# Kernel optimization log

Hardware: AMD Instinct MI355X
Metric: run time of the kernel (lower is better)

The kernel has to match this reference:

```python
import jax, jax.numpy as jnp
import numpy as np

B, C, L = 8, 256, 1024
N_HEAD = 8
GROUPS = 32
EPS = 1e-5


def group_norm(x, gamma, beta):
    # x: [B, C, L]
    b, c, l = x.shape
    xg = x.reshape(b, GROUPS, (c // GROUPS) * l)
    mu = xg.mean(-1, keepdims=True)
    var = xg.var(-1, keepdims=True)
    xg = (xg - mu) / jnp.sqrt(var + EPS)
    x = xg.reshape(b, c, l)
    return x * gamma[None, :, None] + beta[None, :, None]


def conv1d(x, w, b=None, groups=1):
    # x: [B,C,L], w: [O, I/groups, K]
    k = w.shape[-1]
    pad = (k - 1) // 2
    y = jax.lax.conv_general_dilated(
        x, w, window_strides=(1,), padding=[(pad, pad)],
        dimension_numbers=('NCH', 'OIH', 'NCH'),
        feature_group_count=groups)
    if b is not None:
        y = y + b[None, :, None]
    return y


def setup_inputs() -> dict:
    key = jax.random.key(0)
    ks = jax.random.split(key, 8)
    x = jax.random.normal(ks[0], (B, C, L), dtype=jnp.float32)
    gamma = jnp.ones((C,), jnp.float32)
    beta = jnp.zeros((C,), jnp.float32)
    # depthwise conv: torch weight [C,1,3], kaiming_normal fan_in=1*3
    dw_w = jax.random.normal(ks[1], (C, 1, 3), jnp.float32) * np.sqrt(2.0 / 3.0)
    # qkv 1x1 conv: [3C, C, 1], kaiming fan_in=C
    qkv_w = jax.random.normal(ks[2], (3 * C, C, 1), jnp.float32) * np.sqrt(2.0 / C)
    qkv_b = jnp.zeros((3 * C,), jnp.float32)
    out_w = jax.random.normal(ks[3], (C, C, 1), jnp.float32) * np.sqrt(2.0 / C)
    out_b = jnp.zeros((C,), jnp.float32)
    return {"x": x, "gamma": gamma, "beta": beta, "dw_w": dw_w,
            "qkv_w": qkv_w, "qkv_b": qkv_b, "out_w": out_w, "out_b": out_b}


def reference(x, gamma, beta, dw_w, qkv_w, qkv_b, out_w, out_b):
    b, c, l = x.shape
    head_dim = c // N_HEAD
    h = group_norm(x, gamma, beta)
    h = conv1d(h, dw_w, groups=c)                 # depthwise k=3
    qkv = conv1d(h, qkv_w, qkv_b)                 # [B, 3C, L]
    qkv = qkv.reshape(b, N_HEAD, head_dim * 3, l)
    q, k, v = jnp.split(qkv, 3, axis=2)           # each [B, H, D, L]
    attn = jnp.einsum('bhdl,bhdL->bhlL', q, k) / jnp.sqrt(jnp.float32(c))
    attn = jax.nn.softmax(attn, axis=-1)
    o = jnp.einsum('bhlL,bhdL->bhdl', attn, v).reshape(b, c, l)
    o = conv1d(o, out_w, out_b)
    return o + x
```

## Files before the change

kernel.cpp:

```cpp
#include <hip/hip_runtime.h>
#include <hip/hip_bf16.h>

#define B_ 8
#define C_ 256
#define L_ 1024
#define NH_ 8
#define EPS_ 1e-5f

typedef __attribute__((ext_vector_type(8))) _Float16 half8;
typedef __attribute__((ext_vector_type(2))) __fp16 fp16x2;
typedef __attribute__((ext_vector_type(4))) float f32x4;

static __device__ inline ushort f2h(float f) {
  union { _Float16 h; ushort u; } c;
  c.h = (_Float16)f;
  return c.u;
}

static __device__ inline uint pkh(float a, float b) {
  union { fp16x2 v; uint u; } c;
  c.v = __builtin_amdgcn_cvt_pkrtz(a, b);
  return c.u;
}

__global__ __launch_bounds__(512) void gnw_kernel(
    const float* __restrict__ x, const float* __restrict__ gamma,
    const float* __restrict__ beta, const float* __restrict__ dw,
    const float4* __restrict__ qw, const float4* __restrict__ ow,
    uint2* __restrict__ wq, uint2* __restrict__ wo_,
    ushort* __restrict__ ht) {
  __shared__ float hn[8 * L_];
  __shared__ float ws0[8], ws1[8];
  int t = threadIdx.x;
  if (blockIdx.x < 128) {
    int id = blockIdx.x * 512 + t;
    float4 v;
    uint2* dst;
    if (id < 49152) { v = qw[id]; dst = wq + id; }
    else { v = ow[id - 49152]; dst = wo_ + (id - 49152); }
    *dst = make_uint2(pkh(v.x, v.y), pkh(v.z, v.w));
    return;
  }
  int blk = blockIdx.x - 128;
  int b = blk >> 5, g = blk & 31;
  const size_t base = ((size_t)(b * C_ + g * 8)) * L_;

  float s = 0.f, ss = 0.f;
  float vals[16];
#pragma unroll
  for (int i = 0; i < 16; ++i) {
    int e = t + 512 * i;
    float v = x[base + e];
    vals[i] = v;
    s += v; ss += v * v;
  }
#pragma unroll
  for (int off = 32; off >= 1; off >>= 1) {
    s  += __shfl_xor(s, off);
    ss += __shfl_xor(ss, off);
  }
  int wave = t >> 6;
  if ((t & 63) == 0) { ws0[wave] = s; ws1[wave] = ss; }
  __syncthreads();
  s = 0.f; ss = 0.f;
#pragma unroll
  for (int i = 0; i < 8; ++i) { s += ws0[i]; ss += ws1[i]; }
  float mean = s * (1.f / 8192.f);
  float var = ss * (1.f / 8192.f) - mean * mean;
  float rstd = rsqrtf(var + EPS_);

#pragma unroll
  for (int i = 0; i < 16; ++i) {
    int e = t + 512 * i;
    int c = g * 8 + (i >> 1);
    float sc = gamma[c] * rstd;
    hn[e] = (vals[i] - mean) * sc + beta[c];
  }
  __syncthreads();
  float r[16];
#pragma unroll
  for (int i = 0; i < 16; ++i) {
    int e = t + 512 * i;
    int l = e & 1023;
    int c = g * 8 + (i >> 1);
    float w0 = dw[c * 3 + 0], w1 = dw[c * 3 + 1], w2 = dw[c * 3 + 2];
    float a = (l > 0) ? hn[e - 1] : 0.f;
    float m = hn[e];
    float z = (l < 1023) ? hn[e + 1] : 0.f;
    r[i] = w0 * a + w1 * m + w2 * z;
  }
#pragma unroll
  for (int li = 0; li < 2; ++li) {
    int l = t + 512 * li;
    uint4 pk;
    pk.x = pkh(r[0 + li],  r[2 + li]);
    pk.y = pkh(r[4 + li],  r[6 + li]);
    pk.z = pkh(r[8 + li],  r[10 + li]);
    pk.w = pkh(r[12 + li], r[14 + li]);
    *(uint4*)(ht + (((size_t)(b * 32 + g)) * L_ + l) * 8) = pk;
  }
}

__global__ __launch_bounds__(256) void qkv_fused_kernel(
    const ushort* __restrict__ Xt, const ushort* __restrict__ Wb,
    const float* __restrict__ bias, ushort* __restrict__ qt,
    ushort* __restrict__ kt, ushort* __restrict__ vb) {
  int bx = blockIdx.x, head = blockIdx.y, b = blockIdx.z;
  int bh = b * 8 + head;
  int t = threadIdx.x;
  int w = t >> 6, l = t & 63;
  int g = l >> 4, ln = l & 15;
  int wl = w >> 1, wo = w & 1;
  int lbase = bx * 128 + wl * 64;

  const ushort* xb = Xt + (size_t)b * (32 * L_ * 8);
  const ushort* wp = Wb + (size_t)(head * 96 + wo * 48) * 256;

  f32x4 acc[4][3];
#pragma unroll
  for (int ml = 0; ml < 4; ++ml)
#pragma unroll
    for (int nn = 0; nn < 3; ++nn) acc[ml][nn] = (f32x4){0.f, 0.f, 0.f, 0.f};

  for (int c0 = 0; c0 < 256; c0 += 32) {
    half8 af[4], bf[3];
#pragma unroll
    for (int ml = 0; ml < 4; ++ml)
      af[ml] = *(const half8*)(xb +
          (((size_t)((c0 >> 3) + g)) * L_ + lbase + 16 * ml + ln) * 8);
#pragma unroll
    for (int nn = 0; nn < 3; ++nn)
      bf[nn] = *(const half8*)(wp + (size_t)(16 * nn + ln) * 256 + c0 + 8 * g);
#pragma unroll
    for (int ml = 0; ml < 4; ++ml)
#pragma unroll
      for (int nn = 0; nn < 3; ++nn)
        acc[ml][nn] = __builtin_amdgcn_mfma_f32_16x16x32_f16(af[ml], bf[nn], acc[ml][nn], 0, 0, 0);
  }

#pragma unroll
  for (int nn = 0; nn < 3; ++nn) {
    float bs = bias[head * 96 + wo * 48 + 16 * nn + ln];
#pragma unroll
    for (int ml = 0; ml < 4; ++ml)
#pragma unroll
      for (int r = 0; r < 4; ++r) acc[ml][nn][r] += bs;
  }

  __shared__ ushort tr[5120];
  const float QSC = 0.0625f * 1.44269504f;

  for (int rk = 0; rk < 2; ++rk) {
    float sc = rk ? 1.f : QSC;
    __syncthreads();
#pragma unroll
    for (int nn = 0; nn < 3; ++nn) {
      int ocl0 = wo * 48 + 16 * nn;
      if (ocl0 >= rk * 32 && ocl0 < rk * 32 + 32) {
        int d = ocl0 - rk * 32 + ln;
#pragma unroll
        for (int ml = 0; ml < 4; ++ml) {
          int lrow = wl * 64 + 16 * ml + 4 * g;
#pragma unroll
          for (int r = 0; r < 4; ++r)
            tr[(lrow + r) * 40 + d] = f2h(acc[ml][nn][r] * sc);
        }
      }
    }
    __syncthreads();
    {
      int row = t >> 1, half = t & 1;
      uint4 v0 = *(const uint4*)&tr[row * 40 + half * 16];
      uint4 v1 = *(const uint4*)&tr[row * 40 + half * 16 + 8];
      ushort* dst = (rk ? kt : qt) +
                    ((size_t)bh * L_ + bx * 128 + row) * 32 + half * 16;
      *(uint4*)dst = v0;
      *(uint4*)(dst + 8) = v1;
    }
  }

  __syncthreads();
  if (wo == 1) {
#pragma unroll
    for (int nn = 1; nn < 3; ++nn) {
      int d = 16 * (nn - 1) + ln;
#pragma unroll
      for (int ml = 0; ml < 4; ++ml) {
        int lc = wl * 64 + 16 * ml + 4 * g;
        *(uint2*)&tr[d * 136 + lc] =
            make_uint2(pkh(acc[ml][nn][0], acc[ml][nn][1]),
                       pkh(acc[ml][nn][2], acc[ml][nn][3]));
      }
    }
  }
  __syncthreads();
  {
    int d = t >> 3, s0 = t & 7;
    ushort* vdst = vb + ((size_t)bh * 32 + d) * L_ + bx * 128;
#pragma unroll
    for (int c = 0; c < 2; ++c) {
      int ch = s0 + 8 * c;
      int jj = ch >> 2, gg = ch & 3;
      uint2 lo = *(const uint2*)&tr[d * 136 + 32 * jj + 4 * gg];
      uint2 hi = *(const uint2*)&tr[d * 136 + 32 * jj + 16 + 4 * gg];
      *(uint4*)(vdst + 32 * jj + 8 * gg) = make_uint4(lo.x, lo.y, hi.x, hi.y);
    }
  }
}

__global__ __launch_bounds__(256) void outconv_kernel(
    const ushort* __restrict__ Xt, const ushort* __restrict__ Wb,
    const float* __restrict__ bias, const float* __restrict__ resid,
    float* __restrict__ out) {
  int b = blockIdx.z;
  int t = threadIdx.x;
  int w = t >> 6, l = t & 63;
  int g = l >> 4, ln = l & 15;
  int lbase = blockIdx.x * 128;
  int ocblk = blockIdx.y * 64;
  int ocbase = ocblk + w * 16;

  const ushort* xb = Xt + (size_t)b * (8 * L_ * 32);
  const ushort* wp = Wb + (size_t)ocbase * 256;

  f32x4 acc[8];
#pragma unroll
  for (int ml = 0; ml < 8; ++ml) acc[ml] = (f32x4){0.f, 0.f, 0.f, 0.f};

  for (int c0 = 0; c0 < 256; c0 += 32) {
    half8 af[8];
#pragma unroll
    for (int ml = 0; ml < 8; ++ml)
      af[ml] = *(const half8*)(xb +
          ((size_t)(c0 >> 5) * L_ + lbase + 16 * ml + ln) * 32 + 8 * g);
    half8 bf = *(const half8*)(wp + (size_t)ln * 256 + c0 + 8 * g);
#pragma unroll
    for (int ml = 0; ml < 8; ++ml)
      acc[ml] = __builtin_amdgcn_mfma_f32_16x16x32_f16(af[ml], bf, acc[ml], 0, 0, 0);
  }

  __shared__ float tile[64][132];
  float bs = bias[ocbase + ln];
#pragma unroll
  for (int ml = 0; ml < 8; ++ml) {
    int ll = 16 * ml + 4 * g;
    float4 v = make_float4(acc[ml][0] + bs, acc[ml][1] + bs,
                           acc[ml][2] + bs, acc[ml][3] + bs);
    *(float4*)&tile[w * 16 + ln][ll] = v;
  }
  __syncthreads();
  {
    int ocl = t >> 2, lq = t & 3;
    const float* src = &tile[ocl][lq * 32];
    size_t ob = ((size_t)b * 256 + ocblk + ocl) * L_ + lbase + lq * 32;
#pragma unroll
    for (int i = 0; i < 8; ++i) {
      float4 v = *(const float4*)(src + 4 * i);
      float4 rd = *(const float4*)(resid + ob + 4 * i);
      v.x += rd.x; v.y += rd.y; v.z += rd.z; v.w += rd.w;
      *(float4*)(out + ob + 4 * i) = v;
    }
  }
}

__global__ __launch_bounds__(512) void attn_mfma_kernel(
    const ushort* __restrict__ qt, const ushort* __restrict__ kt,
    const ushort* __restrict__ vb, ushort* __restrict__ ot) {
  const int id = blockIdx.x;
  const int bh = ((id & 7) << 3) | (id >> 6);
  const int qtile = (id >> 3) & 7;
  const int t = threadIdx.x;
  const int w = t >> 6, l = t & 63;
  const int g = l >> 4, ln = l & 15;
  const int q0b = qtile * 128;
  const int q0 = q0b + w * 16;

  __shared__ __align__(16) ushort smem[18944];

  const ushort* qbase = qt + (size_t)bh * (L_ * 32);
  const ushort* kbase = kt + (size_t)bh * (L_ * 32);
  const ushort* vbase = vb + (size_t)bh * (32 * L_);

  const int krow = t >> 2, kchunk = t & 3;
  const ushort* kg = kbase + krow * 32 + kchunk * 8;
  const int kwo = krow * 40 + kchunk * 8;
  const int vrow = t >> 4, vchunk = t & 15;
  const ushort* vg = vbase + (size_t)vrow * L_ + vchunk * 8;
  const int vwo = vrow * 136 + vchunk * 8;

  const f32x4 z4 = {0.f, 0.f, 0.f, 0.f};
  const half8 bq = *(const half8*)(qbase + (size_t)(q0 + ln) * 32 + g * 8);

  union { ushort s[8]; half8 v; } onesu;
#pragma unroll
  for (int i = 0; i < 8; ++i) onesu.s[i] = 0x3C00;
  const half8 ones = onesu.v;

  f32x4 oacc[2] = {z4, z4};
  f32x4 oaccS = z4;

  uint4 ka0, va0;
  ka0 = *(const uint4*)kg;
  va0 = *(const uint4*)vg;
  __builtin_amdgcn_sched_barrier(0);
  *(uint4*)&smem[kwo] = ka0;
  *(uint4*)&smem[10240 + vwo] = va0;
  asm volatile("s_waitcnt lgkmcnt(0)" ::: "memory");
  __builtin_amdgcn_s_barrier();
  __builtin_amdgcn_sched_barrier(0);

  for (int tt = 0; tt < 8; ++tt) {
    const int cur = tt & 1;
    if (tt < 7) {
      ka0 = *(const uint4*)(kg + (tt + 1) * 4096);
      va0 = *(const uint4*)(vg + (tt + 1) * 128);
    }
    __builtin_amdgcn_sched_barrier(0);

    const ushort* Kc = &smem[cur * 5120];
    const ushort* Vc = &smem[10240 + cur * 4352];

    f32x4 sacc[8];
#pragma unroll
    for (int mk = 0; mk < 8; ++mk) {
      half8 ak = *(const half8*)(Kc + (16 * mk + ln) * 40 + g * 8);
      sacc[mk] = __builtin_amdgcn_mfma_f32_16x16x32_f16(ak, bq, z4, 0, 0, 0);
    }

    uint upk[8][2];
#pragma unroll
    for (int mk = 0; mk < 8; ++mk) {
      float e0 = __builtin_amdgcn_exp2f(sacc[mk][0]);
      float e1 = __builtin_amdgcn_exp2f(sacc[mk][1]);
      float e2 = __builtin_amdgcn_exp2f(sacc[mk][2]);
      float e3 = __builtin_amdgcn_exp2f(sacc[mk][3]);
      upk[mk][0] = pkh(e0, e1);
      upk[mk][1] = pkh(e2, e3);
    }

#pragma unroll
    for (int ks = 0; ks < 4; ++ks) {
      union { uint u[4]; half8 v; } pb;
      pb.u[0] = upk[2 * ks][0];     pb.u[1] = upk[2 * ks][1];
      pb.u[2] = upk[2 * ks + 1][0]; pb.u[3] = upk[2 * ks + 1][1];
      oaccS = __builtin_amdgcn_mfma_f32_16x16x32_f16(ones, pb.v, oaccS, 0, 0, 0);
#pragma unroll
      for (int md = 0; md < 2; ++md) {
        half8 av = *(const half8*)(Vc + (16 * md + ln) * 136 + 32 * ks + 8 * g);
        oacc[md] = __builtin_amdgcn_mfma_f32_16x16x32_f16(av, pb.v, oacc[md], 0, 0, 0);
      }
    }

    __builtin_amdgcn_sched_barrier(0);
    if (tt < 7) {
      const int nxt = cur ^ 1;
      *(uint4*)&smem[nxt * 5120 + kwo] = ka0;
      *(uint4*)&smem[10240 + nxt * 4352 + vwo] = va0;
      asm volatile("s_waitcnt lgkmcnt(0)" ::: "memory");
      __builtin_amdgcn_s_barrier();
      __builtin_amdgcn_sched_barrier(0);
    }
  }

  ushort* otile = &smem[0];
  float rl = 1.f / oaccS[0];
  int q_loc = w * 16 + ln;
#pragma unroll
  for (int md = 0; md < 2; ++md) {
    uint2 pk = make_uint2(pkh(oacc[md][0] * rl, oacc[md][1] * rl),
                          pkh(oacc[md][2] * rl, oacc[md][3] * rl));
    *(uint2*)&otile[q_loc * 40 + 16 * md + 4 * g] = pk;
  }
  __syncthreads();
  {
    int row = t >> 2, qu = t & 3;
    uint4 v = *(const uint4*)&otile[row * 40 + qu * 8];
    *(uint4*)(ot + ((size_t)bh * L_ + q0b + row) * 32 + qu * 8) = v;
  }
}

extern "C" void kernel_launch(void* const* d_in, const int* in_sizes, int n_in,
                              void* d_out, int out_size, void* d_ws, size_t ws_size,
                              hipStream_t stream) {
  const float* x      = (const float*)d_in[0];
  const float* gamma  = (const float*)d_in[1];
  const float* beta   = (const float*)d_in[2];
  const float* dw     = (const float*)d_in[3];
  const float* qkv_w  = (const float*)d_in[4];
  const float* qkv_b  = (const float*)d_in[5];
  const float* out_w  = (const float*)d_in[6];
  const float* out_b  = (const float*)d_in[7];
  float* out = (float*)d_out;

  char* ws = (char*)d_ws;
  ushort* ht   = (ushort*)(ws);
  ushort* qtb  = (ushort*)(ws + (16u << 20));
  ushort* ktb  = (ushort*)(ws + (20u << 20));
  ushort* vbb  = (ushort*)(ws + (24u << 20));
  ushort* otb  = (ushort*)(ws);
  ushort* wq   = (ushort*)(ws + (28u << 20));
  ushort* wo   = (ushort*)(ws + (28u << 20) + (512u << 10));

  gnw_kernel<<<384, 512, 0, stream>>>(x, gamma, beta, dw,
                                      (const float4*)qkv_w, (const float4*)out_w,
                                      (uint2*)wq, (uint2*)wo, ht);
  qkv_fused_kernel<<<dim3(8, 8, B_), 256, 0, stream>>>(ht, wq, qkv_b, qtb, ktb, vbb);
  attn_mfma_kernel<<<512, 512, 0, stream>>>(qtb, ktb, vbb, otb);
  outconv_kernel<<<dim3(8, 4, B_), 256, 0, stream>>>(otb, wo, out_b, x, out);
}
```

Before: 53.44 us.

## Split group-norm into stats and apply kernels for more parallelism

```diff
diff --git a/kernel.cpp b/kernel.cpp
--- a/kernel.cpp
+++ b/kernel.cpp
@@ -23,14 +23,11 @@
   return c.u;
 }
 
-__global__ __launch_bounds__(512) void gnw_kernel(
-    const float* __restrict__ x, const float* __restrict__ gamma,
-    const float* __restrict__ beta, const float* __restrict__ dw,
+__global__ __launch_bounds__(512) void gnstats_kernel(
+    const float* __restrict__ x,
     const float4* __restrict__ qw, const float4* __restrict__ ow,
     uint2* __restrict__ wq, uint2* __restrict__ wo_,
-    ushort* __restrict__ ht) {
-  __shared__ float hn[8 * L_];
-  __shared__ float ws0[8], ws1[8];
+    float2* __restrict__ part) {
   int t = threadIdx.x;
   if (blockIdx.x < 128) {
     int id = blockIdx.x * 512 + t;
@@ -41,64 +38,83 @@
     *dst = make_uint2(pkh(v.x, v.y), pkh(v.z, v.w));
     return;
   }
-  int blk = blockIdx.x - 128;
-  int b = blk >> 5, g = blk & 31;
-  const size_t base = ((size_t)(b * C_ + g * 8)) * L_;
+  int sid = blockIdx.x - 128;
+  int G = sid >> 1, h = sid & 1;
+  int b = G >> 5, gg = G & 31;
+  const float4* xb = (const float4*)(x + ((size_t)(b * 256 + gg * 8 + h * 4)) * L_);
 
   float s = 0.f, ss = 0.f;
-  float vals[16];
-#pragma unroll
-  for (int i = 0; i < 16; ++i) {
-    int e = t + 512 * i;
-    float v = x[base + e];
-    vals[i] = v;
-    s += v; ss += v * v;
+#pragma unroll
+  for (int i = 0; i < 2; ++i) {
+    float4 v = xb[t + 512 * i];
+    s += v.x + v.y + v.z + v.w;
+    ss += v.x * v.x + v.y * v.y + v.z * v.z + v.w * v.w;
   }
 #pragma unroll
   for (int off = 32; off >= 1; off >>= 1) {
     s  += __shfl_xor(s, off);
     ss += __shfl_xor(ss, off);
   }
+  __shared__ float ws0[8], ws1[8];
   int wave = t >> 6;
   if ((t & 63) == 0) { ws0[wave] = s; ws1[wave] = ss; }
   __syncthreads();
-  s = 0.f; ss = 0.f;
-#pragma unroll
-  for (int i = 0; i < 8; ++i) { s += ws0[i]; ss += ws1[i]; }
+  if (t == 0) {
+    float as = 0.f, ass = 0.f;
+#pragma unroll
+    for (int i = 0; i < 8; ++i) { as += ws0[i]; ass += ws1[i]; }
+    part[sid] = make_float2(as, ass);
+  }
+}
+
+__global__ __launch_bounds__(256) void gnapply_kernel(
+    const float* __restrict__ x, const float* __restrict__ gamma,
+    const float* __restrict__ beta, const float* __restrict__ dw,
+    const float2* __restrict__ part, ushort* __restrict__ ht) {
+  int j = blockIdx.x;
+  int G = j >> 2, ql = j & 3;
+  int b = G >> 5, gg = G & 31;
+  int l0 = ql * 256;
+  int t = threadIdx.x;
+
+  float2 p0 = part[2 * G], p1 = part[2 * G + 1];
+  float s = p0.x + p1.x, ss = p0.y + p1.y;
   float mean = s * (1.f / 8192.f);
   float var = ss * (1.f / 8192.f) - mean * mean;
   float rstd = rsqrtf(var + EPS_);
 
-#pragma unroll
-  for (int i = 0; i < 16; ++i) {
-    int e = t + 512 * i;
-    int c = g * 8 + (i >> 1);
-    float sc = gamma[c] * rstd;
-    hn[e] = (vals[i] - mean) * sc + beta[c];
-  }
-  __syncthreads();
-  float r[16];
-#pragma unroll
-  for (int i = 0; i < 16; ++i) {
-    int e = t + 512 * i;
-    int l = e & 1023;
-    int c = g * 8 + (i >> 1);
-    float w0 = dw[c * 3 + 0], w1 = dw[c * 3 + 1], w2 = dw[c * 3 + 2];
-    float a = (l > 0) ? hn[e - 1] : 0.f;
-    float m = hn[e];
-    float z = (l < 1023) ? hn[e + 1] : 0.f;
-    r[i] = w0 * a + w1 * m + w2 * z;
-  }
-#pragma unroll
-  for (int li = 0; li < 2; ++li) {
-    int l = t + 512 * li;
-    uint4 pk;
-    pk.x = pkh(r[0 + li],  r[2 + li]);
-    pk.y = pkh(r[4 + li],  r[6 + li]);
-    pk.z = pkh(r[8 + li],  r[10 + li]);
-    pk.w = pkh(r[12 + li], r[14 + li]);
-    *(uint4*)(ht + (((size_t)(b * 32 + g)) * L_ + l) * 8) = pk;
-  }
+  __shared__ float hn[8][264];
+  const float* xg = x + ((size_t)(b * 256 + gg * 8)) * L_;
+#pragma unroll
+  for (int c = 0; c < 8; ++c) {
+    float sc = gamma[gg * 8 + c] * rstd;
+    float bt = beta[gg * 8 + c];
+    {
+      int l = l0 - 1 + t;
+      float v = (l >= 0 && l < L_) ? xg[(size_t)c * L_ + l] : 0.f;
+      hn[c][t] = (l >= 0 && l < L_) ? ((v - mean) * sc + bt) : 0.f;
+    }
+    if (t < 2) {
+      int l = l0 + 255 + t;
+      float v = (l < L_) ? xg[(size_t)c * L_ + l] : 0.f;
+      hn[c][256 + t] = (l < L_) ? ((v - mean) * sc + bt) : 0.f;
+    }
+  }
+  __syncthreads();
+
+  float r[8];
+#pragma unroll
+  for (int c = 0; c < 8; ++c) {
+    int cc = gg * 8 + c;
+    float w0 = dw[cc * 3 + 0], w1 = dw[cc * 3 + 1], w2 = dw[cc * 3 + 2];
+    r[c] = w0 * hn[c][t] + w1 * hn[c][t + 1] + w2 * hn[c][t + 2];
+  }
+  uint4 pk;
+  pk.x = pkh(r[0], r[1]);
+  pk.y = pkh(r[2], r[3]);
+  pk.z = pkh(r[4], r[5]);
+  pk.w = pkh(r[6], r[7]);
+  *(uint4*)(ht + (((size_t)(b * 32 + gg)) * L_ + l0 + t) * 8) = pk;
 }
 
 __global__ __launch_bounds__(256) void qkv_fused_kernel(
@@ -400,10 +416,12 @@
   ushort* otb  = (ushort*)(ws);
   ushort* wq   = (ushort*)(ws + (28u << 20));
   ushort* wo   = (ushort*)(ws + (28u << 20) + (512u << 10));
-
-  gnw_kernel<<<384, 512, 0, stream>>>(x, gamma, beta, dw,
-                                      (const float4*)qkv_w, (const float4*)out_w,
-                                      (uint2*)wq, (uint2*)wo, ht);
+  float2* part = (float2*)(ws + (31u << 20));
+
+  gnstats_kernel<<<640, 512, 0, stream>>>(x, (const float4*)qkv_w,
+                                          (const float4*)out_w,
+                                          (uint2*)wq, (uint2*)wo, part);
+  gnapply_kernel<<<1024, 256, 0, stream>>>(x, gamma, beta, dw, part, ht);
   qkv_fused_kernel<<<dim3(8, 8, B_), 256, 0, stream>>>(ht, wq, qkv_b, qtb, ktb, vbb);
   attn_mfma_kernel<<<512, 512, 0, stream>>>(qtb, ktb, vbb, otb);
   outconv_kernel<<<dim3(8, 4, B_), 256, 0, stream>>>(otb, wo, out_b, x, out);
```

Result: slower. 57.96 us (+8.5%).
